# Kernel optimization log

Hardware: AMD Instinct MI355X
Metric: run time of the kernel (lower is better)

The kernel has to match this reference:

```python
import jax, jax.numpy as jnp
import numpy as np

EMB = 768
HEADS = 12
HEAD_DIM = EMB // HEADS


def setup_inputs() -> dict:
    key = jax.random.key(0)
    k1, k2, k3, k4 = jax.random.split(key, 4)
    x = jax.random.normal(k1, (8, 1024, EMB), dtype=jnp.float32)
    # Dense kernels, TF default glorot-ish scale approximated with small normals
    w_qkv = jax.random.normal(k2, (EMB, 3 * EMB), dtype=jnp.float32) * 0.02
    w_out = jax.random.normal(k3, (EMB, EMB), dtype=jnp.float32) * 0.02
    b_out = jnp.zeros((EMB,), dtype=jnp.float32)
    return {"x": x, "w_qkv": w_qkv, "w_out": w_out, "b_out": b_out}


def reference(x, w_qkv, w_out, b_out):
    B, S, E = x.shape
    qkv = jnp.einsum("bse,ef->bsf", x, w_qkv)                 # [B,S,3E]
    qkv = qkv.reshape(B, S, 3, HEADS, HEAD_DIM)
    qkv = jnp.transpose(qkv, (2, 0, 3, 1, 4))                  # [3,B,H,S,D]
    q, k, v = qkv[0], qkv[1], qkv[2]
    scale = jnp.float32(HEAD_DIM) ** -0.5
    # Blocked loop in source computes exact full (non-causal) attention:
    # every query block attends to all keys -> equivalent to standard SDPA.
    scores = jnp.einsum("bhqd,bhkd->bhqk", q, k) * scale       # [B,H,S,S]
    probs = jax.nn.softmax(scores, axis=-1)
    out = jnp.einsum("bhqk,bhkd->bhqd", probs, v)              # [B,H,S,D]
    out = jnp.transpose(out, (0, 2, 1, 3)).reshape(B, S, E)
    return jnp.einsum("bse,ef->bsf", out, w_out) + b_out
```

## Files before the change

### kernel.cpp

```cpp
#include <hip/hip_runtime.h>

typedef float f32x4 __attribute__((ext_vector_type(4)));
typedef short bf16x8 __attribute__((ext_vector_type(8)));

#define MFMA_BF16(a, b, c) __builtin_amdgcn_mfma_f32_16x16x32_bf16((a), (b), (c), 0, 0, 0)

#define GLDS16(gp, lp) __builtin_amdgcn_global_load_lds( \
    (const __attribute__((address_space(1))) unsigned int*)(gp), \
    (__attribute__((address_space(3))) unsigned int*)(lp), 16, 0, 0)

__device__ __forceinline__ ushort f2bf(float f) {
    unsigned int u = __float_as_uint(f);
    return (ushort)((u + 0x7FFFu + ((u >> 16) & 1u)) >> 16);
}

__device__ __forceinline__ float fexp2(float x) {
#if __has_builtin(__builtin_amdgcn_exp2f)
    return __builtin_amdgcn_exp2f(x);
#else
    return exp2f(x);
#endif
}

__global__ __launch_bounds__(256) void cvt_x_kernel(const float4* __restrict__ src,
                                                    ushort4* __restrict__ dst, int n4) {
    for (int i = blockIdx.x * 256 + threadIdx.x; i < n4; i += gridDim.x * 256) {
        float4 v = src[i];
        ushort4 o;
        o.x = f2bf(v.x); o.y = f2bf(v.y); o.z = f2bf(v.z); o.w = f2bf(v.w);
        dst[i] = o;
    }
}

__global__ __launch_bounds__(256) void tcvt_kernel(const float* __restrict__ src,
                                                   ushort* __restrict__ dst, int K, int N) {
    __shared__ float tile[32][33];
    const int n0 = blockIdx.x * 32, k0 = blockIdx.y * 32;
    const int c = threadIdx.x & 31, rb = threadIdx.x >> 5;
    #pragma unroll
    for (int i = 0; i < 4; ++i)
        tile[i * 8 + rb][c] = src[(size_t)(k0 + i * 8 + rb) * N + n0 + c];
    __syncthreads();
    #pragma unroll
    for (int i = 0; i < 4; ++i) {
        int nr = i * 8 + rb;
        dst[(size_t)(n0 + nr) * K + k0 + c] = f2bf(tile[c][nr]);
    }
}

__global__ __launch_bounds__(256) void gemm_qkv_mfma(
    const ushort* __restrict__ A, const ushort* __restrict__ Bt,
    ushort* __restrict__ Qo, ushort* __restrict__ Ko, ushort* __restrict__ Vo)
{
    __shared__ ushort Al[2][4096];
    __shared__ ushort Bl[2][4096];
    const int tid = threadIdx.x, lane = tid & 63;
    const int wv = tid >> 6, lo = lane & 15, hi = lane >> 4;
    const int wr = wv >> 1, wc = wv & 1;
    const int L = blockIdx.x + 18 * blockIdx.y;
    const int nid = (L & 7) * 144 + (L >> 3);
    const int n0 = (nid % 18) * 128, m0 = (nid / 18) * 128;

    auto stage = [&](int bi, int k0) {
        #pragma unroll
        for (int it = 0; it < 2; ++it) {
            const int p = it * 256 + tid;
            const int row = p >> 2, ch = (p & 3) ^ ((row >> 1) & 3);
            GLDS16(A + (size_t)(m0 + row) * 768 + k0 + ch * 8, &Al[bi][(it * 256 + (tid & 192)) * 8]);
            GLDS16(Bt + (size_t)(n0 + row) * 768 + k0 + ch * 8, &Bl[bi][(it * 256 + (tid & 192)) * 8]);
        }
    };

    f32x4 acc[4][4];
    #pragma unroll
    for (int i = 0; i < 4; ++i)
        #pragma unroll
        for (int j = 0; j < 4; ++j)
            acc[i][j] = (f32x4){0.f, 0.f, 0.f, 0.f};

    const int region = n0 / 768;
    const int h = ((n0 % 768) >> 6) + wc;

    stage(0, 0);
    __syncthreads();

    if (region == 2) {
        for (int kt = 0; kt < 24; ++kt) {
            const int cur = kt & 1;
            if (kt < 23) stage(cur ^ 1, (kt + 1) * 32);
            bf16x8 af[4], bfr[4];
            #pragma unroll
            for (int i = 0; i < 4; ++i) {
                const int ra = wr * 64 + i * 16 + lo;
                af[i] = *(const bf16x8*)&Al[cur][ra * 32 + ((hi ^ ((ra >> 1) & 3)) * 8)];
                const int rb = wc * 64 + i * 16 + lo;
                bfr[i] = *(const bf16x8*)&Bl[cur][rb * 32 + ((hi ^ ((rb >> 1) & 3)) * 8)];
            }
            #pragma unroll
            for (int mi = 0; mi < 4; ++mi)
                #pragma unroll
                for (int nj = 0; nj < 4; ++nj)
                    acc[mi][nj] = MFMA_BF16(af[mi], bfr[nj], acc[mi][nj]);
            __syncthreads();
        }
        #pragma unroll
        for (int mi = 0; mi < 4; ++mi) {
            const int m4 = m0 + wr * 64 + mi * 16 + hi * 4;
            const int b = m4 >> 10, s = m4 & 1023;
            #pragma unroll
            for (int nj = 0; nj < 4; ++nj) {
                const int d = nj * 16 + lo;
                ushort4 pk;
                pk.x = f2bf(acc[mi][nj][0]); pk.y = f2bf(acc[mi][nj][1]);
                pk.z = f2bf(acc[mi][nj][2]); pk.w = f2bf(acc[mi][nj][3]);
                *(ushort4*)&Vo[((size_t)(b * 12 + h) * 64 + d) * 1024 + s] = pk;
            }
        }
    } else {
        for (int kt = 0; kt < 24; ++kt) {
            const int cur = kt & 1;
            if (kt < 23) stage(cur ^ 1, (kt + 1) * 32);
            bf16x8 af[4], bfr[4];
            #pragma unroll
            for (int i = 0; i < 4; ++i) {
                const int ra = wr * 64 + i * 16 + lo;
                af[i] = *(const bf16x8*)&Al[cur][ra * 32 + ((hi ^ ((ra >> 1) & 3)) * 8)];
                const int rb = wc * 64 + i * 16 + lo;
                bfr[i] = *(const bf16x8*)&Bl[cur][rb * 32 + ((hi ^ ((rb >> 1) & 3)) * 8)];
            }
            #pragma unroll
            for (int mi = 0; mi < 4; ++mi)
                #pragma unroll
                for (int nj = 0; nj < 4; ++nj)
                    acc[mi][nj] = MFMA_BF16(bfr[nj], af[mi], acc[mi][nj]);
            __syncthreads();
        }
        ushort* dst = region ? Ko : Qo;
        const float sc = region ? 1.0f : 0.18033688011112042f;
        #pragma unroll
        for (int mi = 0; mi < 4; ++mi) {
            const int s_idx = m0 + wr * 64 + mi * 16 + lo;
            const int b = s_idx >> 10, s = s_idx & 1023;
            const size_t base = ((size_t)(b * 12 + h) * 1024 + s) * 64;
            #pragma unroll
            for (int nj = 0; nj < 4; ++nj) {
                ushort4 pk;
                pk.x = f2bf(acc[mi][nj][0] * sc); pk.y = f2bf(acc[mi][nj][1] * sc);
                pk.z = f2bf(acc[mi][nj][2] * sc); pk.w = f2bf(acc[mi][nj][3] * sc);
                *(ushort4*)&dst[base + nj * 16 + hi * 4] = pk;
            }
        }
    }
}

__global__ __launch_bounds__(256) void attn_mfma_kernel(
    const ushort* __restrict__ Qg, const ushort* __restrict__ Kg,
    const ushort* __restrict__ Vg, ushort* __restrict__ AO)
{
    __shared__ ushort Kl[2][4096];
    __shared__ ushort Vl[2][4096];
    __shared__ ushort Pl[4][32 * 72];

    const int tid = threadIdx.x, lane = tid & 63;
    const int wv = tid >> 6, lo = lane & 15, hi = lane >> 4;
    const int L = blockIdx.x;
    const int xcd = L & 7, g = L >> 3;
    const int qb = g / 12;
    const int bh = xcd * 12 + (g % 12);
    const int b = bh / 12, h = bh % 12;
    const size_t kvbase = (size_t)bh * (1024 * 64);

    bf16x8 qa[2][2];
    const int qrow0 = qb * 128 + wv * 32;
    #pragma unroll
    for (int mi = 0; mi < 2; ++mi)
        #pragma unroll
        for (int ks = 0; ks < 2; ++ks)
            qa[mi][ks] = *(const bf16x8*)&Qg[kvbase + (size_t)(qrow0 + mi * 16 + lo) * 64 + ks * 32 + hi * 8];

    f32x4 o[2][4];
    float lp[2] = {0.f, 0.f};
    #pragma unroll
    for (int mi = 0; mi < 2; ++mi)
        #pragma unroll
        for (int dj = 0; dj < 4; ++dj) o[mi][dj] = (f32x4){0.f, 0.f, 0.f, 0.f};

    auto stage = [&](int bi, int kt) {
        #pragma unroll
        for (int it = 0; it < 2; ++it) {
            const int p = it * 256 + tid;
            const int row = p >> 3, ch = (p & 7) ^ (row & 7);
            GLDS16(Kg + kvbase + (size_t)(kt + row) * 64 + ch * 8, &Kl[bi][(it * 256 + (tid & 192)) * 8]);
        }
        #pragma unroll
        for (int it = 0; it < 2; ++it) {
            const int p = it * 256 + tid;
            const int row = p >> 3, ch = (p & 7) ^ (row & 7);
            GLDS16(Vg + kvbase + (size_t)row * 1024 + kt + ch * 8, &Vl[bi][(it * 256 + (tid & 192)) * 8]);
        }
    };

    stage(0, 0);
    __syncthreads();

    for (int t = 0; t < 16; ++t) {
        const int cur = t & 1;
        if (t < 15) stage(cur ^ 1, (t + 1) * 64);

        f32x4 s[2][4];
        #pragma unroll
        for (int mi = 0; mi < 2; ++mi)
            #pragma unroll
            for (int nj = 0; nj < 4; ++nj) s[mi][nj] = (f32x4){0.f, 0.f, 0.f, 0.f};
        #pragma unroll
        for (int ks = 0; ks < 2; ++ks) {
            bf16x8 kb[4];
            #pragma unroll
            for (int nj = 0; nj < 4; ++nj) {
                const int key = nj * 16 + lo, c = ks * 4 + hi;
                kb[nj] = *(const bf16x8*)&Kl[cur][key * 64 + ((c ^ (key & 7)) * 8)];
            }
            #pragma unroll
            for (int mi = 0; mi < 2; ++mi)
                #pragma unroll
                for (int nj = 0; nj < 4; ++nj)
                    s[mi][nj] = MFMA_BF16(kb[nj], qa[mi][ks], s[mi][nj]);
        }

        #pragma unroll
        for (int mi = 0; mi < 2; ++mi) {
            #pragma unroll
            for (int nj = 0; nj < 4; ++nj) {
                const unsigned int u0 = __float_as_uint(fexp2(s[mi][nj][0]));
                const unsigned int u1 = __float_as_uint(fexp2(s[mi][nj][1]));
                const unsigned int u2 = __float_as_uint(fexp2(s[mi][nj][2]));
                const unsigned int u3 = __float_as_uint(fexp2(s[mi][nj][3]));
                const float t0 = __uint_as_float(u0 & 0xFFFF0000u);
                const float t1 = __uint_as_float(u1 & 0xFFFF0000u);
                const float t2 = __uint_as_float(u2 & 0xFFFF0000u);
                const float t3 = __uint_as_float(u3 & 0xFFFF0000u);
                lp[mi] += (t0 + t1) + (t2 + t3);
                ushort4 pk;
                pk.x = (ushort)(u0 >> 16); pk.y = (ushort)(u1 >> 16);
                pk.z = (ushort)(u2 >> 16); pk.w = (ushort)(u3 >> 16);
                *(ushort4*)&Pl[wv][(mi * 16 + lo) * 72 + nj * 16 + hi * 4] = pk;
            }
        }

        #pragma unroll
        for (int ks = 0; ks < 2; ++ks) {
            bf16x8 pa[2];
            #pragma unroll
            for (int mi = 0; mi < 2; ++mi)
                pa[mi] = *(const bf16x8*)&Pl[wv][(mi * 16 + lo) * 72 + ks * 32 + hi * 8];
            bf16x8 vb[4];
            #pragma unroll
            for (int dj = 0; dj < 4; ++dj) {
                const int d = dj * 16 + lo, c = ks * 4 + hi;
                vb[dj] = *(const bf16x8*)&Vl[cur][d * 64 + ((c ^ (d & 7)) * 8)];
            }
            #pragma unroll
            for (int mi = 0; mi < 2; ++mi)
                #pragma unroll
                for (int dj = 0; dj < 4; ++dj)
                    o[mi][dj] = MFMA_BF16(pa[mi], vb[dj], o[mi][dj]);
        }
        __syncthreads();
    }

    #pragma unroll
    for (int mi = 0; mi < 2; ++mi) {
        float l = lp[mi];
        l += __shfl_xor(l, 16);
        l += __shfl_xor(l, 32);
        #pragma unroll
        for (int r = 0; r < 4; ++r) {
            const float lr = __shfl(l, hi * 4 + r, 16);
            const float rcp = 1.0f / lr;
            const int srow = qrow0 + mi * 16 + hi * 4 + r;
            #pragma unroll
            for (int dj = 0; dj < 4; ++dj)
                AO[((size_t)(b * 1024 + srow)) * 768 + h * 64 + dj * 16 + lo] =
                    f2bf(o[mi][dj][r] * rcp);
        }
    }
}

__global__ __launch_bounds__(256) void gemm_out_mfma(
    const ushort* __restrict__ A, const ushort* __restrict__ Bt,
    const float* __restrict__ bias, float* __restrict__ C)
{
    __shared__ ushort Al[2][4096];
    __shared__ ushort Bl[2][4096];
    const int tid = threadIdx.x, lane = tid & 63;
    const int wv = tid >> 6, lo = lane & 15, hi = lane >> 4;
    const int wr = wv >> 1, wc = wv & 1;
    const int L = blockIdx.x + 6 * blockIdx.y;
    const int nid = (L & 7) * 48 + (L >> 3);
    const int n0 = (nid % 6) * 128, m0 = (nid / 6) * 128;

    auto stage = [&](int bi, int k0) {
        #pragma unroll
        for (int it = 0; it < 2; ++it) {
            const int p = it * 256 + tid;
            const int row = p >> 2, ch = (p & 3) ^ ((row >> 1) & 3);
            GLDS16(A + (size_t)(m0 + row) * 768 + k0 + ch * 8, &Al[bi][(it * 256 + (tid & 192)) * 8]);
            GLDS16(Bt + (size_t)(n0 + row) * 768 + k0 + ch * 8, &Bl[bi][(it * 256 + (tid & 192)) * 8]);
        }
    };

    f32x4 acc[4][4];
    #pragma unroll
    for (int i = 0; i < 4; ++i)
        #pragma unroll
        for (int j = 0; j < 4; ++j)
            acc[i][j] = (f32x4){0.f, 0.f, 0.f, 0.f};

    stage(0, 0);
    __syncthreads();
    for (int kt = 0; kt < 24; ++kt) {
        const int cur = kt & 1;
        if (kt < 23) stage(cur ^ 1, (kt + 1) * 32);
        bf16x8 af[4], bfr[4];
        #pragma unroll
        for (int i = 0; i < 4; ++i) {
            const int ra = wr * 64 + i * 16 + lo;
            af[i] = *(const bf16x8*)&Al[cur][ra * 32 + ((hi ^ ((ra >> 1) & 3)) * 8)];
            const int rb = wc * 64 + i * 16 + lo;
            bfr[i] = *(const bf16x8*)&Bl[cur][rb * 32 + ((hi ^ ((rb >> 1) & 3)) * 8)];
        }
        #pragma unroll
        for (int mi = 0; mi < 4; ++mi)
            #pragma unroll
            for (int nj = 0; nj < 4; ++nj)
                acc[mi][nj] = MFMA_BF16(bfr[nj], af[mi], acc[mi][nj]);
        __syncthreads();
    }

    const int ncol0 = n0 + wc * 64;
    #pragma unroll
    for (int mi = 0; mi < 4; ++mi) {
        const int m = m0 + wr * 64 + mi * 16 + lo;
        #pragma unroll
        for (int nj = 0; nj < 4; ++nj) {
            const int nb = ncol0 + nj * 16 + hi * 4;
            const float4 bv = *reinterpret_cast<const float4*>(&bias[nb]);
            float4 ov;
            ov.x = acc[mi][nj][0] + bv.x; ov.y = acc[mi][nj][1] + bv.y;
            ov.z = acc[mi][nj][2] + bv.z; ov.w = acc[mi][nj][3] + bv.w;
            *reinterpret_cast<float4*>(&C[(size_t)m * 768 + nb]) = ov;
        }
    }
}

extern "C" void kernel_launch(void* const* d_in, const int* in_sizes, int n_in,
                              void* d_out, int out_size, void* d_ws, size_t ws_size,
                              hipStream_t stream) {
    const float* x     = (const float*)d_in[0];
    const float* w_qkv = (const float*)d_in[1];
    const float* w_out = (const float*)d_in[2];
    const float* b_out = (const float*)d_in[3];
    float* out = (float*)d_out;

    (void)in_sizes; (void)n_in; (void)out_size; (void)ws_size;

    ushort* xb   = (ushort*)d_ws;
    ushort* wqbt = xb + 6291456;
    ushort* wobt = wqbt + 1769472;
    ushort* Qs   = wobt + 589824;
    ushort* Ks   = Qs + 6291456;
    ushort* Vt   = Ks + 6291456;
    ushort* AO   = Vt + 6291456;

    cvt_x_kernel<<<2048, 256, 0, stream>>>((const float4*)x, (ushort4*)xb, 1572864);
    tcvt_kernel<<<dim3(72, 24), 256, 0, stream>>>(w_qkv, wqbt, 768, 2304);
    tcvt_kernel<<<dim3(24, 24), 256, 0, stream>>>(w_out, wobt, 768, 768);
    gemm_qkv_mfma<<<dim3(18, 64), 256, 0, stream>>>(xb, wqbt, Qs, Ks, Vt);
    attn_mfma_kernel<<<768, 256, 0, stream>>>(Qs, Ks, Vt, AO);
    gemm_out_mfma<<<dim3(6, 64), 256, 0, stream>>>(AO, wobt, b_out, out);
}
```

Baseline: 131.6 us.

## Fuse prep kernels and restructure QKV GEMM with 256-row tiles and triple buffering

Merges the three fp32-to-bf16 conversion and transpose kernels into a single prep launch, which removes two kernel launches. The QKV GEMM switches to 512-thread blocks covering 256x128 tiles with a K-step of 64 and a new XOR swizzle. It uses three LDS stages, explicit vmcnt waits and raw barriers, so global loads run two stages ahead of the MFMAs. LDS use grows to roughly 144KB per block, which limits occupancy to one block per CU, and the grid shrinks to 576 blocks.

```diff
diff --git a/kernel.cpp b/kernel.cpp
--- a/kernel.cpp
+++ b/kernel.cpp
@@ -22,20 +22,32 @@
 #endif
 }
 
-__global__ __launch_bounds__(256) void cvt_x_kernel(const float4* __restrict__ src,
-                                                    ushort4* __restrict__ dst, int n4) {
-    for (int i = blockIdx.x * 256 + threadIdx.x; i < n4; i += gridDim.x * 256) {
-        float4 v = src[i];
-        ushort4 o;
-        o.x = f2bf(v.x); o.y = f2bf(v.y); o.z = f2bf(v.z); o.w = f2bf(v.w);
-        dst[i] = o;
-    }
-}
-
-__global__ __launch_bounds__(256) void tcvt_kernel(const float* __restrict__ src,
-                                                   ushort* __restrict__ dst, int K, int N) {
+__global__ __launch_bounds__(256) void prep_kernel(
+    const float* __restrict__ x, const float* __restrict__ wq, const float* __restrict__ wo,
+    ushort* __restrict__ xb, ushort* __restrict__ wqbt, ushort* __restrict__ wobt)
+{
     __shared__ float tile[32][33];
-    const int n0 = blockIdx.x * 32, k0 = blockIdx.y * 32;
+    const int bid = blockIdx.x;
+    if (bid < 2048) {
+        const float4* src = (const float4*)x;
+        ushort4* dst = (ushort4*)xb;
+        for (int i = bid * 256 + threadIdx.x; i < 1572864; i += 2048 * 256) {
+            float4 v = src[i];
+            ushort4 o;
+            o.x = f2bf(v.x); o.y = f2bf(v.y); o.z = f2bf(v.z); o.w = f2bf(v.w);
+            dst[i] = o;
+        }
+        return;
+    }
+    const float* src; ushort* dst; int K, N, bx, by;
+    if (bid < 3776) {
+        const int L = bid - 2048;
+        src = wq; dst = wqbt; K = 768; N = 2304; bx = L % 72; by = L / 72;
+    } else {
+        const int L = bid - 3776;
+        src = wo; dst = wobt; K = 768; N = 768; bx = L % 24; by = L / 24;
+    }
+    const int n0 = bx * 32, k0 = by * 32;
     const int c = threadIdx.x & 31, rb = threadIdx.x >> 5;
     #pragma unroll
     for (int i = 0; i < 4; ++i)
@@ -48,26 +60,35 @@
     }
 }
 
-__global__ __launch_bounds__(256) void gemm_qkv_mfma(
+__global__ __launch_bounds__(512) void gemm_qkv_mfma(
     const ushort* __restrict__ A, const ushort* __restrict__ Bt,
     ushort* __restrict__ Qo, ushort* __restrict__ Ko, ushort* __restrict__ Vo)
 {
-    __shared__ ushort Al[2][4096];
-    __shared__ ushort Bl[2][4096];
+    __shared__ ushort Al[3][16384];
+    __shared__ ushort Bl[3][8192];
     const int tid = threadIdx.x, lane = tid & 63;
     const int wv = tid >> 6, lo = lane & 15, hi = lane >> 4;
     const int wr = wv >> 1, wc = wv & 1;
-    const int L = blockIdx.x + 18 * blockIdx.y;
-    const int nid = (L & 7) * 144 + (L >> 3);
-    const int n0 = (nid % 18) * 128, m0 = (nid / 18) * 128;
-
-    auto stage = [&](int bi, int k0) {
+    const int L = blockIdx.x;
+    const int nid = (L & 7) * 72 + (L >> 3);
+    const int n0 = (nid % 18) * 128, m0 = (nid / 18) * 256;
+
+    auto stageA = [&](int bi, int k0) {
+        #pragma unroll
+        for (int it = 0; it < 4; ++it) {
+            const int p = it * 512 + tid;
+            const int row = p >> 3, ch = (p & 7) ^ (row & 7);
+            GLDS16(A + (size_t)(m0 + row) * 768 + k0 + ch * 8,
+                   &Al[bi][(it * 512 + (tid & 448)) * 8]);
+        }
+    };
+    auto stageB = [&](int bi, int k0) {
         #pragma unroll
         for (int it = 0; it < 2; ++it) {
-            const int p = it * 256 + tid;
-            const int row = p >> 2, ch = (p & 3) ^ ((row >> 1) & 3);
-            GLDS16(A + (size_t)(m0 + row) * 768 + k0 + ch * 8, &Al[bi][(it * 256 + (tid & 192)) * 8]);
-            GLDS16(Bt + (size_t)(n0 + row) * 768 + k0 + ch * 8, &Bl[bi][(it * 256 + (tid & 192)) * 8]);
+            const int p = it * 512 + tid;
+            const int row = p >> 3, ch = (p & 7) ^ (row & 7);
+            GLDS16(Bt + (size_t)(n0 + row) * 768 + k0 + ch * 8,
+                   &Bl[bi][(it * 512 + (tid & 448)) * 8]);
         }
     };
 
@@ -81,28 +102,48 @@
     const int region = n0 / 768;
     const int h = ((n0 % 768) >> 6) + wc;
 
-    stage(0, 0);
-    __syncthreads();
-
-    if (region == 2) {
-        for (int kt = 0; kt < 24; ++kt) {
-            const int cur = kt & 1;
-            if (kt < 23) stage(cur ^ 1, (kt + 1) * 32);
+    stageA(0, 0);  stageB(0, 0);
+    stageA(1, 64); stageB(1, 64);
+
+    int cur = 0;
+    for (int t = 0; t < 12; ++t) {
+        if (t < 11) asm volatile("s_waitcnt vmcnt(6)" ::: "memory");
+        else        asm volatile("s_waitcnt vmcnt(0)" ::: "memory");
+        __builtin_amdgcn_s_barrier();
+        asm volatile("" ::: "memory");
+        if (t + 2 < 12) {
+            const int nb = cur ? cur - 1 : 2;
+            stageA(nb, (t + 2) * 64);
+            stageB(nb, (t + 2) * 64);
+        }
+        #pragma unroll
+        for (int ks = 0; ks < 2; ++ks) {
             bf16x8 af[4], bfr[4];
             #pragma unroll
             for (int i = 0; i < 4; ++i) {
                 const int ra = wr * 64 + i * 16 + lo;
-                af[i] = *(const bf16x8*)&Al[cur][ra * 32 + ((hi ^ ((ra >> 1) & 3)) * 8)];
+                af[i] = *(const bf16x8*)&Al[cur][ra * 64 + (((ks * 4 + hi) ^ (ra & 7)) * 8)];
                 const int rb = wc * 64 + i * 16 + lo;
-                bfr[i] = *(const bf16x8*)&Bl[cur][rb * 32 + ((hi ^ ((rb >> 1) & 3)) * 8)];
-            }
-            #pragma unroll
-            for (int mi = 0; mi < 4; ++mi)
+                bfr[i] = *(const bf16x8*)&Bl[cur][rb * 64 + (((ks * 4 + hi) ^ (rb & 7)) * 8)];
+            }
+            if (region == 2) {
                 #pragma unroll
-                for (int nj = 0; nj < 4; ++nj)
-                    acc[mi][nj] = MFMA_BF16(af[mi], bfr[nj], acc[mi][nj]);
-            __syncthreads();
-        }
+                for (int mi = 0; mi < 4; ++mi)
+                    #pragma unroll
+                    for (int nj = 0; nj < 4; ++nj)
+                        acc[mi][nj] = MFMA_BF16(af[mi], bfr[nj], acc[mi][nj]);
+            } else {
+                #pragma unroll
+                for (int mi = 0; mi < 4; ++mi)
+                    #pragma unroll
+                    for (int nj = 0; nj < 4; ++nj)
+                        acc[mi][nj] = MFMA_BF16(bfr[nj], af[mi], acc[mi][nj]);
+            }
+        }
+        cur = cur == 2 ? 0 : cur + 1;
+    }
+
+    if (region == 2) {
         #pragma unroll
         for (int mi = 0; mi < 4; ++mi) {
             const int m4 = m0 + wr * 64 + mi * 16 + hi * 4;
@@ -117,24 +158,6 @@
             }
         }
     } else {
-        for (int kt = 0; kt < 24; ++kt) {
-            const int cur = kt & 1;
-            if (kt < 23) stage(cur ^ 1, (kt + 1) * 32);
-            bf16x8 af[4], bfr[4];
-            #pragma unroll
-            for (int i = 0; i < 4; ++i) {
-                const int ra = wr * 64 + i * 16 + lo;
-                af[i] = *(const bf16x8*)&Al[cur][ra * 32 + ((hi ^ ((ra >> 1) & 3)) * 8)];
-                const int rb = wc * 64 + i * 16 + lo;
-                bfr[i] = *(const bf16x8*)&Bl[cur][rb * 32 + ((hi ^ ((rb >> 1) & 3)) * 8)];
-            }
-            #pragma unroll
-            for (int mi = 0; mi < 4; ++mi)
-                #pragma unroll
-                for (int nj = 0; nj < 4; ++nj)
-                    acc[mi][nj] = MFMA_BF16(bfr[nj], af[mi], acc[mi][nj]);
-            __syncthreads();
-        }
         ushort* dst = region ? Ko : Qo;
         const float sc = region ? 1.0f : 0.18033688011112042f;
         #pragma unroll
@@ -372,10 +395,8 @@
     ushort* Vt   = Ks + 6291456;
     ushort* AO   = Vt + 6291456;
 
-    cvt_x_kernel<<<2048, 256, 0, stream>>>((const float4*)x, (ushort4*)xb, 1572864);
-    tcvt_kernel<<<dim3(72, 24), 256, 0, stream>>>(w_qkv, wqbt, 768, 2304);
-    tcvt_kernel<<<dim3(24, 24), 256, 0, stream>>>(w_out, wobt, 768, 768);
-    gemm_qkv_mfma<<<dim3(18, 64), 256, 0, stream>>>(xb, wqbt, Qs, Ks, Vt);
+    prep_kernel<<<4352, 256, 0, stream>>>(x, w_qkv, w_out, xb, wqbt, wobt);
+    gemm_qkv_mfma<<<576, 512, 0, stream>>>(xb, wqbt, Qs, Ks, Vt);
     attn_mfma_kernel<<<768, 256, 0, stream>>>(Qs, Ks, Vt, AO);
     gemm_out_mfma<<<dim3(6, 64), 256, 0, stream>>>(AO, wobt, b_out, out);
 }
```

After: 134.6 us. 2.3% more time.
